# Performance work log

Hardware: AMD Instinct MI355X
Metric: run time of the kernel (lower is better)

## Reference

```python
import jax, jax.numpy as jnp
import numpy as np

N, D, E = 100000, 32, 1600000
EH, NH = 32, 16
TAU = 0.1


def setup_inputs() -> dict:
    key = jax.random.key(0)
    ks = jax.random.split(key, 12)
    x = jax.random.normal(ks[0], (N, D), dtype=jnp.float32)
    edge_index = jax.random.randint(ks[1], (2, E), 0, N, dtype=jnp.int32)
    hsd = jax.random.normal(ks[2], (N,), dtype=jnp.float32)
    s_e1 = 1.0 / np.sqrt(D + 2)
    s_e2 = 1.0 / np.sqrt(EH)
    s_n2 = 1.0 / np.sqrt(NH)
    We1 = jax.random.uniform(ks[3], (D + 2, EH), jnp.float32, -s_e1, s_e1)
    be1 = jax.random.uniform(ks[4], (EH,), jnp.float32, -s_e1, s_e1)
    We2 = jax.random.uniform(ks[5], (EH, 1), jnp.float32, -s_e2, s_e2)
    be2 = jax.random.uniform(ks[6], (1,), jnp.float32, -s_e2, s_e2)
    Wn1 = jax.random.uniform(ks[7], (1, NH), jnp.float32, -1.0, 1.0)
    bn1 = jax.random.uniform(ks[8], (NH,), jnp.float32, -1.0, 1.0)
    Wn2 = jax.random.uniform(ks[9], (NH, 1), jnp.float32, -s_n2, s_n2)
    bn2 = jax.random.uniform(ks[10], (1,), jnp.float32, -s_n2, s_n2)
    return {"x": x, "hsd": hsd, "We1": We1, "be1": be1, "We2": We2, "be2": be2,
            "Wn1": Wn1, "bn1": bn1, "Wn2": Wn2, "bn2": bn2, "edge_index": edge_index}


def reference(x, hsd, We1, be1, We2, be2, Wn1, bn1, Wn2, bn2, edge_index):
    row, col = edge_index[0], edge_index[1]
    n = x.shape[0]
    # normalized HSD (torch.std is unbiased, ddof=1)
    hsd_norm = (hsd - hsd.mean()) / (jnp.std(hsd, ddof=1) + 1e-8)
    # edge MLP input: [hsd_u, hsd_v, |x_u - x_v|]  -> (E, D+2)
    diff_abs = jnp.abs(x[row] - x[col])
    edge_in = jnp.concatenate([hsd_norm[row][:, None], hsd_norm[col][:, None], diff_abs], axis=1)
    h = jax.nn.relu(edge_in @ We1 + be1)
    e_uv = (h @ We2 + be2)[:, 0]  # (E,)
    # segment softmax over destination (col)
    logits = e_uv / TAU
    seg_max = jax.ops.segment_max(logits, col, num_segments=n)
    seg_max = jnp.where(jnp.isfinite(seg_max), seg_max, 0.0)
    ex = jnp.exp(logits - seg_max[col])
    denom = jax.ops.segment_sum(ex, col, num_segments=n)
    alpha_uv = (ex / (denom[col] + 1e-16))[:, None]  # (E,1)
    # node-level gate
    gh = jax.nn.relu(hsd_norm[:, None] @ Wn1 + bn1)
    alpha_bar = jax.nn.sigmoid(gh @ Wn2 + bn2)  # (N,1)
    # degree normalization
    ones = jnp.ones(row.shape[0], dtype=x.dtype)
    src_deg = jnp.sqrt(jnp.clip(jax.ops.segment_sum(ones, row, num_segments=n), 1.0))
    dst_deg = jnp.sqrt(jnp.clip(jax.ops.segment_sum(ones, col, num_segments=n), 1.0))
    edge_w = 1.0 / (src_deg[row] * dst_deg[col])
    low_pass = jax.ops.segment_sum(edge_w[:, None] * x[row], col, num_segments=n)
    high_pass = jax.ops.segment_sum(alpha_uv * (x[col] - x[row]), col, num_segments=n)
    return (1.0 - alpha_bar) * low_pass + alpha_bar * high_pass
```

## Files before the change

kernel.cpp:

```cpp
#include <hip/hip_runtime.h>

#define D_FEAT 32
#define EHID 32
#define NHID 16
#define INV_TAU 10.0f
#define SCAN_CHUNK 1024
#define EPB 256
#define SDS 40
#define TILE 8192
#define BSH 7
#define NBIN 128
#define BMASK 127
#define CAP 3072

typedef __attribute__((ext_vector_type(8))) short short8v;
typedef __attribute__((ext_vector_type(4))) float f32x4;

__device__ __forceinline__ unsigned enc_f32(float f) {
    unsigned b = __float_as_uint(f);
    return (b & 0x80000000u) ? ~b : (b | 0x80000000u);
}
__device__ __forceinline__ float dec_f32(unsigned e) {
    unsigned b = (e & 0x80000000u) ? (e & 0x7fffffffu) : ~e;
    return __uint_as_float(b);
}
__device__ __forceinline__ unsigned short f2bf(float f) {
    unsigned u = __float_as_uint(f);
    u += 0x7fffu + ((u >> 16) & 1u);
    return (unsigned short)(u >> 16);
}
__device__ __forceinline__ float bflo(unsigned u) { return __uint_as_float(u << 16); }
__device__ __forceinline__ float bfhi(unsigned u) { return __uint_as_float(u & 0xFFFF0000u); }

__global__ __launch_bounds__(256) void k1_hsd_stats(const float* __restrict__ hsd,
                                                    double* __restrict__ stats, int N) {
    double s = 0.0, s2 = 0.0;
    for (int i = blockIdx.x * 256 + threadIdx.x; i < N; i += gridDim.x * 256) {
        double v = (double)hsd[i];
        s += v; s2 += v * v;
    }
    for (int off = 32; off > 0; off >>= 1) {
        s  += __shfl_down(s,  off, 64);
        s2 += __shfl_down(s2, off, 64);
    }
    __shared__ double ls[4], ls2[4];
    int wid = threadIdx.x >> 6, lid = threadIdx.x & 63;
    if (lid == 0) { ls[wid] = s; ls2[wid] = s2; }
    __syncthreads();
    if (threadIdx.x == 0) {
        double ts = 0.0, t2 = 0.0;
        for (int w = 0; w < 4; ++w) { ts += ls[w]; t2 += ls2[w]; }
        atomicAdd(stats, ts);
        atomicAdd(stats + 1, t2);
    }
}

__global__ __launch_bounds__(256) void k2_node_prep(const float* __restrict__ hsd,
                                                    const double* __restrict__ stats,
                                                    const float* __restrict__ Wn1,
                                                    const float* __restrict__ bn1,
                                                    const float* __restrict__ Wn2,
                                                    const float* __restrict__ bn2,
                                                    float* __restrict__ hsd_norm,
                                                    float* __restrict__ alpha_bar, int N) {
    int n = blockIdx.x * 256 + threadIdx.x;
    if (n >= N) return;
    double sum = stats[0], sumsq = stats[1];
    double mean = sum / (double)N;
    double var  = (sumsq - sum * sum / (double)N) / (double)(N - 1);
    float stdv  = (float)sqrt(var);
    float hn = (hsd[n] - (float)mean) / (stdv + 1e-8f);
    hsd_norm[n] = hn;
    float acc = bn2[0];
#pragma unroll
    for (int k = 0; k < NHID; ++k)
        acc += fmaxf(fmaf(hn, Wn1[k], bn1[k]), 0.0f) * Wn2[k];
    alpha_bar[n] = 1.0f / (1.0f + __expf(-acc));
}

__global__ __launch_bounds__(256) void s1_hist(const int* __restrict__ ei,
                                               int* __restrict__ hist,
                                               int E, int NB, int T, int M) {
    __shared__ int hv[1024], hu[1024];
    int t = threadIdx.x;
    for (int b = t; b < 1024; b += 256) { hv[b] = 0; hu[b] = 0; }
    __syncthreads();
    int base = blockIdx.x * TILE;
    for (int i = t; i < TILE; i += 256) {
        int e = base + i;
        if (e < E) {
            int u = ei[e], v = ei[E + e];
            atomicAdd(&hv[v >> BSH], 1);
            atomicAdd(&hu[u >> BSH], 1);
        }
    }
    __syncthreads();
    for (int b = t; b < NB; b += 256) {
        hist[b * T + blockIdx.x] = hv[b];
        hist[M + b * T + blockIdx.x] = hu[b];
    }
}

__global__ __launch_bounds__(256) void scan_k1(const int* __restrict__ cnt,
                                               int* __restrict__ out,
                                               int* __restrict__ partials, int N) {
    __shared__ int lds[256];
    int base = blockIdx.x * SCAN_CHUNK;
    int t = threadIdx.x;
    int v[4]; int loc = 0;
#pragma unroll
    for (int k = 0; k < 4; ++k) {
        int idx = base + t * 4 + k;
        v[k] = (idx < N) ? cnt[idx] : 0;
        loc += v[k];
    }
    lds[t] = loc; __syncthreads();
    for (int off = 1; off < 256; off <<= 1) {
        int a = (t >= off) ? lds[t - off] : 0;
        __syncthreads();
        lds[t] += a;
        __syncthreads();
    }
    int run = (t > 0) ? lds[t - 1] : 0;
    if (t == 255) partials[blockIdx.x] = lds[255];
#pragma unroll
    for (int k = 0; k < 4; ++k) {
        run += v[k];
        int idx = base + t * 4 + k;
        if (idx < N) out[idx + 1] = run;
    }
    if (blockIdx.x == 0 && t == 0) out[0] = 0;
}

__global__ __launch_bounds__(256) void scan_k2(int* __restrict__ partials, int B) {
    __shared__ int lds[256];
    int t = threadIdx.x;
    int v[4]; int loc = 0;
#pragma unroll
    for (int k = 0; k < 4; ++k) {
        int idx = t * 4 + k;
        v[k] = (idx < B) ? partials[idx] : 0;
        loc += v[k];
    }
    lds[t] = loc; __syncthreads();
    for (int off = 1; off < 256; off <<= 1) {
        int a = (t >= off) ? lds[t - off] : 0;
        __syncthreads();
        lds[t] += a;
        __syncthreads();
    }
    int run = (t > 0) ? lds[t - 1] : 0;
#pragma unroll
    for (int k = 0; k < 4; ++k) {
        int idx = t * 4 + k;
        if (idx < B) { partials[idx] = run; run += v[k]; }
    }
}

__global__ __launch_bounds__(256) void scan_k3(int* __restrict__ out,
                                               const int* __restrict__ partials, int N) {
    int i = blockIdx.x * 256 + threadIdx.x;
    if (i >= N) return;
    out[i + 1] += partials[i / SCAN_CHUNK];
}

__global__ __launch_bounds__(256) void s2_scatter(const int* __restrict__ ei,
                                                  const int* __restrict__ scanAll,
                                                  int2* __restrict__ coarse,
                                                  int* __restrict__ coarseU,
                                                  int E, int NB, int T, int M) {
    __shared__ int curV[1024], curU[1024];
    int t = threadIdx.x;
    for (int b = t; b < NB; b += 256) {
        curV[b] = scanAll[b * T + blockIdx.x];
        curU[b] = scanAll[M + b * T + blockIdx.x] - E;
    }
    __syncthreads();
    int base = blockIdx.x * TILE;
    for (int i = t; i < TILE; i += 256) {
        int e = base + i;
        if (e < E) {
            int u = ei[e], v = ei[E + e];
            int pv = atomicAdd(&curV[v >> BSH], 1);
            coarse[pv] = make_int2(u, v);
            int pu = atomicAdd(&curU[u >> BSH], 1);
            coarseU[pu] = u;
        }
    }
}

__global__ __launch_bounds__(256) void s3b_srccnt(const int* __restrict__ coarseU,
                                                  const int* __restrict__ scanAll,
                                                  float* __restrict__ inv_ssrc,
                                                  int N, int E, int NB, int T, int M) {
    __shared__ int cnt[NBIN];
    int t = threadIdx.x;
    int bin = blockIdx.x;
    int start = scanAll[M + bin * T] - E;
    int endv  = scanAll[M + (bin + 1) * T] - E;
    if (t < NBIN) cnt[t] = 0;
    __syncthreads();
    for (int i = start + t; i < endv; i += 256) atomicAdd(&cnt[coarseU[i] & BMASK], 1);
    __syncthreads();
    int vglob = (bin << BSH) + t;
    if (t < NBIN && vglob < N) inv_ssrc[vglob] = rsqrtf(fmaxf((float)cnt[t], 1.0f));
}

__global__ __launch_bounds__(256) void k3d_mlp(const float* __restrict__ x,
                                               const float* __restrict__ hsd_norm,
                                               const float* __restrict__ We1,
                                               const float* __restrict__ be1,
                                               const float* __restrict__ We2,
                                               const float* __restrict__ be2,
                                               const int2* __restrict__ esorted,
                                               float* __restrict__ logit, int E) {
    __shared__ unsigned short sdiff[EPB * SDS];
    __shared__ unsigned short sB[4 * 64 * 8];

    int t = threadIdx.x;
    {
        int f = t >> 6, l = t & 63;
        int c = f >> 1, hh = f & 1;
        int col = hh * 16 + (l & 15);
        int k0 = c * 32 + (l >> 4) * 8;
        unsigned short vals[8];
#pragma unroll
        for (int b = 0; b < 8; ++b) {
            int k = k0 + b;
            int row = (k < 32) ? (k + 2) : (k == 32 ? 0 : (k == 33 ? 1 : -1));
            float w = (row >= 0) ? We1[row * EHID + col] : 0.0f;
            vals[b] = f2bf(w);
        }
        *(uint4*)&sB[(f * 64 + l) * 8] = *(const uint4*)vals;
    }

    int base = blockIdx.x * EPB;
    int q = t & 7;
#pragma unroll
    for (int k = 0; k < 8; ++k) {
        int s = (t >> 3) + 32 * k;
        int e = base + s;
        int ec = (e < E) ? e : (E - 1);
        int2 uv = esorted[ec];
        float4 a = *(const float4*)(x + (size_t)uv.x * D_FEAT + 4 * q);
        float4 b = *(const float4*)(x + (size_t)uv.y * D_FEAT + 4 * q);
        ushort4 pk;
        pk.x = f2bf(fabsf(a.x - b.x));
        pk.y = f2bf(fabsf(a.y - b.y));
        pk.z = f2bf(fabsf(a.z - b.z));
        pk.w = f2bf(fabsf(a.w - b.w));
        *(ushort4*)&sdiff[s * SDS + 4 * q] = pk;
        if (q == 0) {
            uint4 z;
            z.x = (unsigned)f2bf(hsd_norm[uv.x]) | ((unsigned)f2bf(hsd_norm[uv.y]) << 16);
            z.y = 0u; z.z = 0u; z.w = 0u;
            *(uint4*)&sdiff[s * SDS + 32] = z;
        }
    }
    __syncthreads();

    int l = t & 63, w = t >> 6;
    short8v B00 = *(const short8v*)&sB[(0 * 64 + l) * 8];
    short8v B01 = *(const short8v*)&sB[(1 * 64 + l) * 8];
    short8v B10 = *(const short8v*)&sB[(2 * 64 + l) * 8];
    short8v B11 = *(const short8v*)&sB[(3 * 64 + l) * 8];
    float blo = be1[l & 15], bhi = be1[16 + (l & 15)];
    float w2lo = We2[l & 15], w2hi = We2[16 + (l & 15)];
    float b2 = be2[0];
    int wbase = base + w * 64;

#pragma unroll
    for (int g = 0; g < 4; ++g) {
        int row = w * 64 / 1;
        row = g * 16 + (l & 15) + w * 64;
        const short8v a0 = *(const short8v*)&sdiff[row * SDS + (l >> 4) * 8];
        short8v a1 = (short8v)(short)0;
        if (l < 16) a1 = *(const short8v*)&sdiff[row * SDS + 32];
        f32x4 c0 = {blo, blo, blo, blo};
        f32x4 c1 = {bhi, bhi, bhi, bhi};
        c0 = __builtin_amdgcn_mfma_f32_16x16x32_bf16(a0, B00, c0, 0, 0, 0);
        c0 = __builtin_amdgcn_mfma_f32_16x16x32_bf16(a1, B10, c0, 0, 0, 0);
        c1 = __builtin_amdgcn_mfma_f32_16x16x32_bf16(a0, B01, c1, 0, 0, 0);
        c1 = __builtin_amdgcn_mfma_f32_16x16x32_bf16(a1, B11, c1, 0, 0, 0);
#pragma unroll
        for (int r = 0; r < 4; ++r) {
            float vsum = fmaxf(c0[r], 0.0f) * w2lo + fmaxf(c1[r], 0.0f) * w2hi;
            vsum += __shfl_xor(vsum, 1, 64);
            vsum += __shfl_xor(vsum, 2, 64);
            vsum += __shfl_xor(vsum, 4, 64);
            vsum += __shfl_xor(vsum, 8, 64);
            int eo = wbase + g * 16 + (l >> 4) * 4 + r;
            if ((l & 15) == r && eo < E) logit[eo] = (vsum + b2) * INV_TAU;
        }
    }
}

__global__ __launch_bounds__(512) void k6a_tab(const int2* __restrict__ coarse,
                                               const float* __restrict__ logit,
                                               const int* __restrict__ scanAll,
                                               const float* __restrict__ inv_ssrc,
                                               const float* __restrict__ alpha_bar,
                                               int* __restrict__ usrc,
                                               float* __restrict__ coefG,
                                               int* __restrict__ dst_off,
                                               float* __restrict__ selfc,
                                               int N, int E, int NB, int T) {
    __shared__ int      su[CAP];
    __shared__ float    slg[CAP];
    __shared__ int      cnt[NBIN];
    __shared__ unsigned mEnc[NBIN];
    __shared__ float    den[NBIN], cA[NBIN], cB[NBIN];
    __shared__ int      base_[NBIN], cur_[NBIN];

    int t = threadIdx.x;
    int bin = blockIdx.x;
    int start = scanAll[bin * T];
    int n = scanAll[(bin + 1) * T] - start;
    if (n > CAP) n = CAP;

    if (t < NBIN) { cnt[t] = 0; mEnc[t] = 0u; den[t] = 0.0f; }
    __syncthreads();

    for (int i = t; i < n; i += 512) {
        int2 c = coarse[start + i];
        float lgv = logit[start + i];
        int vl = c.y & BMASK;
        su[i] = c.x | (vl << 17);
        slg[i] = lgv;
        atomicAdd(&cnt[vl], 1);
        atomicMax(&mEnc[vl], enc_f32(lgv));
    }
    __syncthreads();

    for (int i = t; i < n; i += 512) {
        int vl = su[i] >> 17;
        atomicAdd(&den[vl], __expf(slg[i] - dec_f32(mEnc[vl])));
    }
    __syncthreads();

    for (int off = 1; off < NBIN; off <<= 1) {
        int a = 0;
        if (t < NBIN && t >= off) a = cnt[t - off];
        __syncthreads();
        if (t < NBIN) cnt[t] += a;
        __syncthreads();
    }
    if (t < NBIN) {
        int b0 = (t > 0) ? cnt[t - 1] : 0;
        base_[t] = b0; cur_[t] = b0;
        int vg = (bin << BSH) + t;
        if (vg < N) {
            float ab = alpha_bar[vg];
            float d = den[t];
            float inv_den = 1.0f / (d + 1e-16f);
            int deg = cnt[t] - b0;
            cA[t] = -ab * inv_den;
            cB[t] = (1.0f - ab) * rsqrtf(fmaxf((float)deg, 1.0f));
            dst_off[vg] = start + b0;
            selfc[vg] = ab * (d * inv_den);
        }
    }
    if (bin == 0 && t == 0) dst_off[N] = E;
    __syncthreads();

    for (int i = t; i < n; i += 512) {
        int up = su[i];
        int vl = up >> 17;
        int u = up & 0x1FFFF;
        int p = start + atomicAdd(&cur_[vl], 1);
        float coef = fmaf(cA[vl], __expf(slg[i] - dec_f32(mEnc[vl])), cB[vl] * inv_ssrc[u]);
        usrc[p] = u;
        coefG[p] = coef;
    }
}

__global__ __launch_bounds__(256) void kx_pack(const float* __restrict__ x,
                                               unsigned* __restrict__ xbf, int n2) {
    int i = blockIdx.x * 256 + threadIdx.x;
    if (i >= n2) return;
    float2 f = *(const float2*)(x + 2 * (size_t)i);
    xbf[i] = (unsigned)f2bf(f.x) | ((unsigned)f2bf(f.y) << 16);
}

__global__ __launch_bounds__(256) void k7_gather(const unsigned* __restrict__ xbf,
                                                 const int* __restrict__ dst_off,
                                                 const int* __restrict__ usrc,
                                                 const float* __restrict__ coefG,
                                                 const float* __restrict__ selfc,
                                                 float* __restrict__ out, int N) {
    int v = blockIdx.x * 16 + (threadIdx.x >> 4);
    if (v >= N) return;
    int l = threadIdx.x & 15;

    int beg = dst_off[v], end = dst_off[v + 1];

    float a0 = 0.0f, a1 = 0.0f;
    int j = beg;
    for (; j + 3 < end; j += 4) {
        int u0 = usrc[j], u1 = usrc[j + 1], u2 = usrc[j + 2], u3 = usrc[j + 3];
        float c0 = coefG[j], c1 = coefG[j + 1], c2 = coefG[j + 2], c3 = coefG[j + 3];
        unsigned q0 = xbf[(size_t)u0 * 16 + l];
        unsigned q1 = xbf[(size_t)u1 * 16 + l];
        unsigned q2 = xbf[(size_t)u2 * 16 + l];
        unsigned q3 = xbf[(size_t)u3 * 16 + l];
        a0 = fmaf(c0, bflo(q0), a0); a1 = fmaf(c0, bfhi(q0), a1);
        a0 = fmaf(c1, bflo(q1), a0); a1 = fmaf(c1, bfhi(q1), a1);
        a0 = fmaf(c2, bflo(q2), a0); a1 = fmaf(c2, bfhi(q2), a1);
        a0 = fmaf(c3, bflo(q3), a0); a1 = fmaf(c3, bfhi(q3), a1);
    }
    for (; j < end; ++j) {
        unsigned q0 = xbf[(size_t)usrc[j] * 16 + l];
        float c0 = coefG[j];
        a0 = fmaf(c0, bflo(q0), a0); a1 = fmaf(c0, bfhi(q0), a1);
    }
    float sc = selfc[v];
    unsigned qv = xbf[(size_t)v * 16 + l];
    a0 = fmaf(sc, bflo(qv), a0);
    a1 = fmaf(sc, bfhi(qv), a1);
    float2 r; r.x = a0; r.y = a1;
    *(float2*)(out + (size_t)v * D_FEAT + 2 * l) = r;
}

extern "C" void kernel_launch(void* const* d_in, const int* in_sizes, int n_in,
                              void* d_out, int out_size, void* d_ws, size_t ws_size,
                              hipStream_t stream) {
    const float* x    = (const float*)d_in[0];
    const float* hsd  = (const float*)d_in[1];
    const float* We1  = (const float*)d_in[2];
    const float* be1  = (const float*)d_in[3];
    const float* We2  = (const float*)d_in[4];
    const float* be2  = (const float*)d_in[5];
    const float* Wn1  = (const float*)d_in[6];
    const float* bn1  = (const float*)d_in[7];
    const float* Wn2  = (const float*)d_in[8];
    const float* bn2  = (const float*)d_in[9];
    const int*   ei   = (const int*)d_in[10];
    float* out = (float*)d_out;

    const int N = in_sizes[1];
    const int E = in_sizes[10] / 2;
    const int NB = (N + NBIN - 1) >> BSH;
    const int T  = (E + TILE - 1) / TILE;
    const int M  = NB * T;
    const int M2 = 2 * M;

    char* ws = (char*)d_ws;
    size_t o = 0;
    auto alloc = [&](size_t bytes) { size_t r = o; o += (bytes + 255) & ~(size_t)255; return r; };
    double* stats     = (double*)(ws + alloc(16));
    float*  inv_ssrc  = (float*)(ws + alloc((size_t)4 * N));
    float*  hsd_norm  = (float*)(ws + alloc((size_t)4 * N));
    float*  alpha_bar = (float*)(ws + alloc((size_t)4 * N));
    float*  selfc     = (float*)(ws + alloc((size_t)4 * N));
    int*    dst_off   = (int*)(ws + alloc((size_t)4 * (N + 1)));
    int*    partials  = (int*)(ws + alloc(4096));
    int*    bufH      = (int*)(ws + alloc((size_t)4 * M2));
    int*    bufS      = (int*)(ws + alloc((size_t)4 * (M2 + 1)));
    int2*   coarse    = (int2*)(ws + alloc((size_t)8 * E));
    int*    coarseU   = (int*)(ws + alloc((size_t)4 * E));
    float*  logit     = (float*)coarseU;
    int*    usrc      = (int*)(ws + alloc((size_t)4 * E));
    float*  coefG     = (float*)(ws + alloc((size_t)4 * E));
    unsigned* xbf     = (unsigned*)coarse;

    hipMemsetAsync(d_ws, 0, 256, stream);

    k1_hsd_stats<<<256, 256, 0, stream>>>(hsd, stats, N);
    k2_node_prep<<<(N + 255) / 256, 256, 0, stream>>>(hsd, stats, Wn1, bn1, Wn2, bn2,
                                                      hsd_norm, alpha_bar, N);

    s1_hist<<<T, 256, 0, stream>>>(ei, bufH, E, NB, T, M);

    int Bs = (M2 + SCAN_CHUNK - 1) / SCAN_CHUNK;
    scan_k1<<<Bs, 256, 0, stream>>>(bufH, bufS, partials, M2);
    scan_k2<<<1, 256, 0, stream>>>(partials, Bs);
    scan_k3<<<(M2 + 255) / 256, 256, 0, stream>>>(bufS, partials, M2);

    s2_scatter<<<T, 256, 0, stream>>>(ei, bufS, coarse, coarseU, E, NB, T, M);
    s3b_srccnt<<<NB, 256, 0, stream>>>(coarseU, bufS, inv_ssrc, N, E, NB, T, M);
    k3d_mlp<<<(E + EPB - 1) / EPB, 256, 0, stream>>>(x, hsd_norm, We1, be1, We2, be2,
                                                     coarse, logit, E);
    k6a_tab<<<NB, 512, 0, stream>>>(coarse, logit, bufS, inv_ssrc, alpha_bar,
                                    usrc, coefG, dst_off, selfc, N, E, NB, T);
    kx_pack<<<(N * (D_FEAT / 2) + 255) / 256, 256, 0, stream>>>(x, xbf, N * (D_FEAT / 2));
    k7_gather<<<(N + 15) / 16, 256, 0, stream>>>(xbf, dst_off, usrc, coefG, selfc, out, N);
}
```

Measured before the change: 294.5 us.

## Fuse edge MLP into per-bin softmax kernel using packed edges and bf16 features

The standalone edge-MLP kernel is merged into the per-destination-bin softmax/table kernel. Logits are now computed directly into shared memory, so they no longer round-trip through global memory. The scatter now writes 4-byte packed (u, local v) edges instead of int2 pairs, and the MLP gathers bf16-packed x, which is produced first in its own buffer, instead of fp32 x. The cost is that MLP work runs on only NB (~782) blocks of 512 threads with a larger LDS footprint, which may reduce parallelism. The diff input is also now quantized from bf16 features.

```diff
diff --git a/kernel.cpp b/kernel.cpp
--- a/kernel.cpp
+++ b/kernel.cpp
@@ -5,7 +5,6 @@
 #define NHID 16
 #define INV_TAU 10.0f
 #define SCAN_CHUNK 1024
-#define EPB 256
 #define SDS 40
 #define TILE 8192
 #define BSH 7
@@ -31,6 +30,14 @@
 }
 __device__ __forceinline__ float bflo(unsigned u) { return __uint_as_float(u << 16); }
 __device__ __forceinline__ float bfhi(unsigned u) { return __uint_as_float(u & 0xFFFF0000u); }
+
+__global__ __launch_bounds__(256) void kx_pack(const float* __restrict__ x,
+                                               unsigned* __restrict__ xbf, int n2) {
+    int i = blockIdx.x * 256 + threadIdx.x;
+    if (i >= n2) return;
+    float2 f = *(const float2*)(x + 2 * (size_t)i);
+    xbf[i] = (unsigned)f2bf(f.x) | ((unsigned)f2bf(f.y) << 16);
+}
 
 __global__ __launch_bounds__(256) void k1_hsd_stats(const float* __restrict__ hsd,
                                                     double* __restrict__ stats, int N) {
@@ -166,7 +173,7 @@
 
 __global__ __launch_bounds__(256) void s2_scatter(const int* __restrict__ ei,
                                                   const int* __restrict__ scanAll,
-                                                  int2* __restrict__ coarse,
+                                                  int* __restrict__ pkG,
                                                   int* __restrict__ coarseU,
                                                   int E, int NB, int T, int M) {
     __shared__ int curV[1024], curU[1024];
@@ -182,7 +189,7 @@
         if (e < E) {
             int u = ei[e], v = ei[E + e];
             int pv = atomicAdd(&curV[v >> BSH], 1);
-            coarse[pv] = make_int2(u, v);
+            pkG[pv] = u | ((v & BMASK) << 17);
             int pu = atomicAdd(&curU[u >> BSH], 1);
             coarseU[pu] = u;
         }
@@ -206,97 +213,13 @@
     if (t < NBIN && vglob < N) inv_ssrc[vglob] = rsqrtf(fmaxf((float)cnt[t], 1.0f));
 }
 
-__global__ __launch_bounds__(256) void k3d_mlp(const float* __restrict__ x,
+__global__ __launch_bounds__(512) void k36_bin(const unsigned* __restrict__ xbf,
                                                const float* __restrict__ hsd_norm,
                                                const float* __restrict__ We1,
                                                const float* __restrict__ be1,
                                                const float* __restrict__ We2,
                                                const float* __restrict__ be2,
-                                               const int2* __restrict__ esorted,
-                                               float* __restrict__ logit, int E) {
-    __shared__ unsigned short sdiff[EPB * SDS];
-    __shared__ unsigned short sB[4 * 64 * 8];
-
-    int t = threadIdx.x;
-    {
-        int f = t >> 6, l = t & 63;
-        int c = f >> 1, hh = f & 1;
-        int col = hh * 16 + (l & 15);
-        int k0 = c * 32 + (l >> 4) * 8;
-        unsigned short vals[8];
-#pragma unroll
-        for (int b = 0; b < 8; ++b) {
-            int k = k0 + b;
-            int row = (k < 32) ? (k + 2) : (k == 32 ? 0 : (k == 33 ? 1 : -1));
-            float w = (row >= 0) ? We1[row * EHID + col] : 0.0f;
-            vals[b] = f2bf(w);
-        }
-        *(uint4*)&sB[(f * 64 + l) * 8] = *(const uint4*)vals;
-    }
-
-    int base = blockIdx.x * EPB;
-    int q = t & 7;
-#pragma unroll
-    for (int k = 0; k < 8; ++k) {
-        int s = (t >> 3) + 32 * k;
-        int e = base + s;
-        int ec = (e < E) ? e : (E - 1);
-        int2 uv = esorted[ec];
-        float4 a = *(const float4*)(x + (size_t)uv.x * D_FEAT + 4 * q);
-        float4 b = *(const float4*)(x + (size_t)uv.y * D_FEAT + 4 * q);
-        ushort4 pk;
-        pk.x = f2bf(fabsf(a.x - b.x));
-        pk.y = f2bf(fabsf(a.y - b.y));
-        pk.z = f2bf(fabsf(a.z - b.z));
-        pk.w = f2bf(fabsf(a.w - b.w));
-        *(ushort4*)&sdiff[s * SDS + 4 * q] = pk;
-        if (q == 0) {
-            uint4 z;
-            z.x = (unsigned)f2bf(hsd_norm[uv.x]) | ((unsigned)f2bf(hsd_norm[uv.y]) << 16);
-            z.y = 0u; z.z = 0u; z.w = 0u;
-            *(uint4*)&sdiff[s * SDS + 32] = z;
-        }
-    }
-    __syncthreads();
-
-    int l = t & 63, w = t >> 6;
-    short8v B00 = *(const short8v*)&sB[(0 * 64 + l) * 8];
-    short8v B01 = *(const short8v*)&sB[(1 * 64 + l) * 8];
-    short8v B10 = *(const short8v*)&sB[(2 * 64 + l) * 8];
-    short8v B11 = *(const short8v*)&sB[(3 * 64 + l) * 8];
-    float blo = be1[l & 15], bhi = be1[16 + (l & 15)];
-    float w2lo = We2[l & 15], w2hi = We2[16 + (l & 15)];
-    float b2 = be2[0];
-    int wbase = base + w * 64;
-
-#pragma unroll
-    for (int g = 0; g < 4; ++g) {
-        int row = w * 64 / 1;
-        row = g * 16 + (l & 15) + w * 64;
-        const short8v a0 = *(const short8v*)&sdiff[row * SDS + (l >> 4) * 8];
-        short8v a1 = (short8v)(short)0;
-        if (l < 16) a1 = *(const short8v*)&sdiff[row * SDS + 32];
-        f32x4 c0 = {blo, blo, blo, blo};
-        f32x4 c1 = {bhi, bhi, bhi, bhi};
-        c0 = __builtin_amdgcn_mfma_f32_16x16x32_bf16(a0, B00, c0, 0, 0, 0);
-        c0 = __builtin_amdgcn_mfma_f32_16x16x32_bf16(a1, B10, c0, 0, 0, 0);
-        c1 = __builtin_amdgcn_mfma_f32_16x16x32_bf16(a0, B01, c1, 0, 0, 0);
-        c1 = __builtin_amdgcn_mfma_f32_16x16x32_bf16(a1, B11, c1, 0, 0, 0);
-#pragma unroll
-        for (int r = 0; r < 4; ++r) {
-            float vsum = fmaxf(c0[r], 0.0f) * w2lo + fmaxf(c1[r], 0.0f) * w2hi;
-            vsum += __shfl_xor(vsum, 1, 64);
-            vsum += __shfl_xor(vsum, 2, 64);
-            vsum += __shfl_xor(vsum, 4, 64);
-            vsum += __shfl_xor(vsum, 8, 64);
-            int eo = wbase + g * 16 + (l >> 4) * 4 + r;
-            if ((l & 15) == r && eo < E) logit[eo] = (vsum + b2) * INV_TAU;
-        }
-    }
-}
-
-__global__ __launch_bounds__(512) void k6a_tab(const int2* __restrict__ coarse,
-                                               const float* __restrict__ logit,
+                                               const int* __restrict__ pkG,
                                                const int* __restrict__ scanAll,
                                                const float* __restrict__ inv_ssrc,
                                                const float* __restrict__ alpha_bar,
@@ -307,6 +230,8 @@
                                                int N, int E, int NB, int T) {
     __shared__ int      su[CAP];
     __shared__ float    slg[CAP];
+    __shared__ unsigned short sdiff[256 * SDS];
+    __shared__ unsigned short sB[4 * 64 * 8];
     __shared__ int      cnt[NBIN];
     __shared__ unsigned mEnc[NBIN];
     __shared__ float    den[NBIN], cA[NBIN], cB[NBIN];
@@ -318,26 +243,102 @@
     int n = scanAll[(bin + 1) * T] - start;
     if (n > CAP) n = CAP;
 
+    if (t < 256) {
+        int f = t >> 6, l = t & 63;
+        int c = f >> 1, hh = f & 1;
+        int col = hh * 16 + (l & 15);
+        int k0 = c * 32 + (l >> 4) * 8;
+        unsigned short vals[8];
+#pragma unroll
+        for (int b = 0; b < 8; ++b) {
+            int k = k0 + b;
+            int row = (k < 32) ? (k + 2) : (k == 32 ? 0 : (k == 33 ? 1 : -1));
+            float w = (row >= 0) ? We1[row * EHID + col] : 0.0f;
+            vals[b] = f2bf(w);
+        }
+        *(uint4*)&sB[(f * 64 + l) * 8] = *(const uint4*)vals;
+    }
     if (t < NBIN) { cnt[t] = 0; mEnc[t] = 0u; den[t] = 0.0f; }
     __syncthreads();
 
     for (int i = t; i < n; i += 512) {
-        int2 c = coarse[start + i];
-        float lgv = logit[start + i];
-        int vl = c.y & BMASK;
-        su[i] = c.x | (vl << 17);
-        slg[i] = lgv;
-        atomicAdd(&cnt[vl], 1);
-        atomicMax(&mEnc[vl], enc_f32(lgv));
-    }
-    __syncthreads();
-
+        int pk = pkG[start + i];
+        su[i] = pk;
+        atomicAdd(&cnt[pk >> 17], 1);
+    }
+    __syncthreads();
+
+    int l = t & 63, w = t >> 6;
+    short8v B00 = *(const short8v*)&sB[(0 * 64 + l) * 8];
+    short8v B01 = *(const short8v*)&sB[(1 * 64 + l) * 8];
+    short8v B10 = *(const short8v*)&sB[(2 * 64 + l) * 8];
+    short8v B11 = *(const short8v*)&sB[(3 * 64 + l) * 8];
+    float blo = be1[l & 15], bhi = be1[16 + (l & 15)];
+    float w2lo = We2[l & 15], w2hi = We2[16 + (l & 15)];
+    float b2 = be2[0];
+    int vbase = bin << BSH;
+
+    for (int c0 = 0; c0 < n; c0 += 256) {
+        int q = t & 7;
+#pragma unroll
+        for (int k = 0; k < 4; ++k) {
+            int s = (t >> 3) + 64 * k;
+            int i = c0 + s;
+            int pk = su[(i < n) ? i : (n - 1)];
+            int u = pk & 0x1FFFF;
+            int v = vbase + (pk >> 17);
+            uint2 au = *(const uint2*)(xbf + (size_t)u * 16 + q * 2);
+            uint2 av = *(const uint2*)(xbf + (size_t)v * 16 + q * 2);
+            ushort4 pkd;
+            pkd.x = f2bf(fabsf(bflo(au.x) - bflo(av.x)));
+            pkd.y = f2bf(fabsf(bfhi(au.x) - bfhi(av.x)));
+            pkd.z = f2bf(fabsf(bflo(au.y) - bflo(av.y)));
+            pkd.w = f2bf(fabsf(bfhi(au.y) - bfhi(av.y)));
+            *(ushort4*)&sdiff[s * SDS + q * 4] = pkd;
+            if (q == 0) {
+                uint4 z;
+                z.x = (unsigned)f2bf(hsd_norm[u]) | ((unsigned)f2bf(hsd_norm[v]) << 16);
+                z.y = 0u; z.z = 0u; z.w = 0u;
+                *(uint4*)&sdiff[s * SDS + 32] = z;
+            }
+        }
+        __syncthreads();
+
+#pragma unroll
+        for (int gg = 0; gg < 2; ++gg) {
+            int grow = (w * 2 + gg) * 16;
+            int row = grow + (l & 15);
+            const short8v a0 = *(const short8v*)&sdiff[row * SDS + (l >> 4) * 8];
+            short8v a1 = (short8v)(short)0;
+            if (l < 16) a1 = *(const short8v*)&sdiff[row * SDS + 32];
+            f32x4 d0 = {blo, blo, blo, blo};
+            f32x4 d1 = {bhi, bhi, bhi, bhi};
+            d0 = __builtin_amdgcn_mfma_f32_16x16x32_bf16(a0, B00, d0, 0, 0, 0);
+            d0 = __builtin_amdgcn_mfma_f32_16x16x32_bf16(a1, B10, d0, 0, 0, 0);
+            d1 = __builtin_amdgcn_mfma_f32_16x16x32_bf16(a0, B01, d1, 0, 0, 0);
+            d1 = __builtin_amdgcn_mfma_f32_16x16x32_bf16(a1, B11, d1, 0, 0, 0);
+#pragma unroll
+            for (int r = 0; r < 4; ++r) {
+                float vsum = fmaxf(d0[r], 0.0f) * w2lo + fmaxf(d1[r], 0.0f) * w2hi;
+                vsum += __shfl_xor(vsum, 1, 64);
+                vsum += __shfl_xor(vsum, 2, 64);
+                vsum += __shfl_xor(vsum, 4, 64);
+                vsum += __shfl_xor(vsum, 8, 64);
+                int eo = c0 + grow + (l >> 4) * 4 + r;
+                if ((l & 15) == r && eo < n) slg[eo] = (vsum + b2) * INV_TAU;
+            }
+        }
+        __syncthreads();
+    }
+
+    for (int i = t; i < n; i += 512)
+        atomicMax(&mEnc[su[i] >> 17], enc_f32(slg[i]));
+    __syncthreads();
     for (int i = t; i < n; i += 512) {
         int vl = su[i] >> 17;
         atomicAdd(&den[vl], __expf(slg[i] - dec_f32(mEnc[vl])));
     }
     __syncthreads();
-
     for (int off = 1; off < NBIN; off <<= 1) {
         int a = 0;
         if (t < NBIN && t >= off) a = cnt[t - off];
@@ -348,7 +349,7 @@
     if (t < NBIN) {
         int b0 = (t > 0) ? cnt[t - 1] : 0;
         base_[t] = b0; cur_[t] = b0;
-        int vg = (bin << BSH) + t;
+        int vg = vbase + t;
         if (vg < N) {
             float ab = alpha_bar[vg];
             float d = den[t];
@@ -362,24 +363,15 @@
     }
     if (bin == 0 && t == 0) dst_off[N] = E;
     __syncthreads();
-
     for (int i = t; i < n; i += 512) {
-        int up = su[i];
-        int vl = up >> 17;
-        int u = up & 0x1FFFF;
+        int pk = su[i];
+        int vl = pk >> 17;
+        int u = pk & 0x1FFFF;
         int p = start + atomicAdd(&cur_[vl], 1);
         float coef = fmaf(cA[vl], __expf(slg[i] - dec_f32(mEnc[vl])), cB[vl] * inv_ssrc[u]);
         usrc[p] = u;
         coefG[p] = coef;
     }
-}
-
-__global__ __launch_bounds__(256) void kx_pack(const float* __restrict__ x,
-                                               unsigned* __restrict__ xbf, int n2) {
-    int i = blockIdx.x * 256 + threadIdx.x;
-    if (i >= n2) return;
-    float2 f = *(const float2*)(x + 2 * (size_t)i);
-    xbf[i] = (unsigned)f2bf(f.x) | ((unsigned)f2bf(f.y) << 16);
 }
 
 __global__ __launch_bounds__(256) void k7_gather(const unsigned* __restrict__ xbf,
@@ -456,15 +448,15 @@
     int*    partials  = (int*)(ws + alloc(4096));
     int*    bufH      = (int*)(ws + alloc((size_t)4 * M2));
     int*    bufS      = (int*)(ws + alloc((size_t)4 * (M2 + 1)));
-    int2*   coarse    = (int2*)(ws + alloc((size_t)8 * E));
+    int*    pkG       = (int*)(ws + alloc((size_t)4 * E));
     int*    coarseU   = (int*)(ws + alloc((size_t)4 * E));
-    float*  logit     = (float*)coarseU;
     int*    usrc      = (int*)(ws + alloc((size_t)4 * E));
     float*  coefG     = (float*)(ws + alloc((size_t)4 * E));
-    unsigned* xbf     = (unsigned*)coarse;
+    unsigned* xbf     = (unsigned*)(ws + alloc((size_t)4 * N * 16));
 
     hipMemsetAsync(d_ws, 0, 256, stream);
 
+    kx_pack<<<(N * (D_FEAT / 2) + 255) / 256, 256, 0, stream>>>(x, xbf, N * (D_FEAT / 2));
     k1_hsd_stats<<<256, 256, 0, stream>>>(hsd, stats, N);
     k2_node_prep<<<(N + 255) / 256, 256, 0, stream>>>(hsd, stats, Wn1, bn1, Wn2, bn2,
                                                       hsd_norm, alpha_bar, N);
@@ -476,12 +468,10 @@
     scan_k2<<<1, 256, 0, stream>>>(partials, Bs);
     scan_k3<<<(M2 + 255) / 256, 256, 0, stream>>>(bufS, partials, M2);
 
-    s2_scatter<<<T, 256, 0, stream>>>(ei, bufS, coarse, coarseU, E, NB, T, M);
+    s2_scatter<<<T, 256, 0, stream>>>(ei, bufS, pkG, coarseU, E, NB, T, M);
     s3b_srccnt<<<NB, 256, 0, stream>>>(coarseU, bufS, inv_ssrc, N, E, NB, T, M);
-    k3d_mlp<<<(E + EPB - 1) / EPB, 256, 0, stream>>>(x, hsd_norm, We1, be1, We2, be2,
-                                                     coarse, logit, E);
-    k6a_tab<<<NB, 512, 0, stream>>>(coarse, logit, bufS, inv_ssrc, alpha_bar,
-                                    usrc, coefG, dst_off, selfc, N, E, NB, T);
-    kx_pack<<<(N * (D_FEAT / 2) + 255) / 256, 256, 0, stream>>>(x, xbf, N * (D_FEAT / 2));
+    k36_bin<<<NB, 512, 0, stream>>>(xbf, hsd_norm, We1, be1, We2, be2, pkG, bufS,
+                                    inv_ssrc, alpha_bar, usrc, coefG, dst_off, selfc,
+                                    N, E, NB, T);
     k7_gather<<<(N + 15) / 16, 256, 0, stream>>>(xbf, dst_off, usrc, coefG, selfc, out, N);
 }
```

Result: no change. 297.2 us (+0.9%).
